# Kernel tuning notes

Measured on AMD Instinct MI355X. Metric: run time of the kernel, lower is better.

The kernel has to match this reference:

```python
import jax, jax.numpy as jnp
import numpy as np

N = 100000
E = 1600000
C_IN = 32
C_OUT = 64
DIM = 3
K = 2 ** DIM  # kernel_size=2 per pseudo-dim, degree=1 => 8 kernel slots
EPS = 1e-5

_BITS = jnp.asarray(np.array([[(c >> d) & 1 for d in range(DIM)] for c in range(K)], dtype=np.float32))  # [K,DIM]


def spline_basis(edge_attr):
    # edge_attr: [E,DIM] pseudo coords in [0,1]. kernel_size=2, degree=1 =>
    # per-dim linear basis (1-u, u); product over dims gives [E,K].
    u = edge_attr[:, None, :]            # [E,1,DIM]
    b = _BITS[None, :, :]                # [1,K,DIM]
    return jnp.prod(b * u + (1.0 - b) * (1.0 - u), axis=-1)  # [E,K]


def spline_conv(x, edge_index, edge_attr, W, W_root):
    # SplineConv with aggr='mean', root_weight=True, bias=False.
    src, dst = edge_index[0], edge_index[1]
    basis = spline_basis(edge_attr)                      # [E,K]
    x_j = x[src]                                         # [E,C_in] gather
    msg = jnp.einsum('ek,ei,kio->eo', basis, x_j, W)     # [E,C_out]
    agg = jax.ops.segment_sum(msg, dst, num_segments=N)  # [N,C_out] scatter-add
    cnt = jax.ops.segment_sum(jnp.ones((msg.shape[0],), msg.dtype), dst, num_segments=N)
    agg = agg / jnp.maximum(cnt, 1.0)[:, None]           # mean aggregation
    return agg + x @ W_root


def batch_norm(x, gamma, beta):
    mu = jnp.mean(x, axis=0)
    var = jnp.var(x, axis=0)
    return (x - mu) * jax.lax.rsqrt(var + EPS) * gamma + beta


def setup_inputs() -> dict:
    key = jax.random.key(0)
    ks = jax.random.split(key, 12)
    x = jax.random.normal(ks[0], (N, C_IN), jnp.float32)
    edge_index = jax.random.randint(ks[1], (2, E), 0, N, jnp.int32)
    edge_attr = jax.random.uniform(ks[2], (E, DIM), jnp.float32)
    s1 = 1.0 / np.sqrt(C_IN)
    s2 = 1.0 / np.sqrt(C_OUT)
    return {
        'x': x,
        'edge_index': edge_index,
        'edge_attr': edge_attr,
        'W1': jax.random.normal(ks[3], (K, C_IN, C_OUT), jnp.float32) * s1,
        'root1': jax.random.normal(ks[4], (C_IN, C_OUT), jnp.float32) * s1,
        'g1': jnp.ones((C_OUT,), jnp.float32),
        'b1': jnp.zeros((C_OUT,), jnp.float32),
        'W2': jax.random.normal(ks[5], (K, C_OUT, C_OUT), jnp.float32) * s2,
        'root2': jax.random.normal(ks[6], (C_OUT, C_OUT), jnp.float32) * s2,
        'g2': jnp.ones((C_OUT,), jnp.float32),
        'b2': jnp.zeros((C_OUT,), jnp.float32),
        'W_skip': jax.random.normal(ks[7], (C_IN, C_OUT), jnp.float32) * s1,
        'g_skip': jnp.ones((C_OUT,), jnp.float32),
        'b_skip': jnp.zeros((C_OUT,), jnp.float32),
    }


def reference(x, edge_index, edge_attr, W1, root1, g1, b1, W2, root2, g2, b2, W_skip, g_skip, b_skip):
    # ConvBlock: SplineConv -> BN -> elu
    h = spline_conv(x, edge_index, edge_attr, W1, root1)
    h = jax.nn.elu(batch_norm(h, g1, b1))
    # ConvBlockWithSkip: SplineConv -> BN; Linear skip -> BN; elu(sum)
    skip = batch_norm(x @ W_skip, g_skip, b_skip)
    h2 = batch_norm(spline_conv(h, edge_index, edge_attr, W2, root2), g2, b2)
    return jax.nn.elu(h2 + skip)
```

## Files before the change

### kernel.cpp

```cpp
#include <hip/hip_runtime.h>
#include <cstdint>

#define BN_EPS 1e-5f

typedef __attribute__((ext_vector_type(8))) short bf16x8;
typedef __attribute__((ext_vector_type(4))) float f32x4;
typedef __attribute__((ext_vector_type(2))) float f32x2;
typedef __attribute__((ext_vector_type(4))) unsigned int u32x4;
typedef unsigned int uint32;
typedef unsigned short u16;

__device__ inline u16 f2bf(float f) {
  unsigned int b = __float_as_uint(f);
  b += 0x7FFFu + ((b >> 16) & 1u);
  return (u16)(b >> 16);
}
__device__ inline float bf2f(u16 u) { return __uint_as_float((unsigned int)u << 16); }

__global__ __launch_bounds__(256) void prep(const float* __restrict__ W1,
                                            const float* __restrict__ root1,
                                            const float* __restrict__ Wskip,
                                            const float* __restrict__ W2,
                                            const float* __restrict__ root2,
                                            u16* __restrict__ B1t, u16* __restrict__ B2t,
                                            const float* __restrict__ x,
                                            u16* __restrict__ xbf, uint32* __restrict__ x8,
                                            int total8) {
  int idx = blockIdx.x * 256 + threadIdx.x;
  if (idx < 128 * 288) {
    int n = idx / 288, a = idx % 288;
    float v;
    if (a < 256) {
      int i = a >> 3, k = a & 7;
      v = (n < 64) ? W1[k * 2048 + i * 64 + n] : 0.f;
    } else {
      int i = a - 256;
      v = (n < 64) ? root1[i * 64 + n] : Wskip[i * 64 + (n - 64)];
    }
    B1t[idx] = f2bf(v);
  } else if (idx < 128 * 288 + 64 * 576) {
    int j = idx - 128 * 288;
    int n = j / 576, a = j % 576;
    float v;
    if (a < 512) {
      int i = a >> 3, k = a & 7;
      v = W2[k * 4096 + i * 64 + n];
    } else {
      v = root2[(a - 512) * 64 + n];
    }
    B2t[j] = f2bf(v);
  }
  if (idx < total8) {
    const float4* xp = (const float4*)x;
    float4 a = xp[2 * idx], b = xp[2 * idx + 1];
    union { u16 s[8]; uint4 u; } p;
    p.s[0] = f2bf(a.x); p.s[1] = f2bf(a.y); p.s[2] = f2bf(a.z); p.s[3] = f2bf(a.w);
    p.s[4] = f2bf(b.x); p.s[5] = f2bf(b.y); p.s[6] = f2bf(b.z); p.s[7] = f2bf(b.w);
    ((uint4*)xbf)[idx] = p.u;
    uint32 w0 = (uint32)__builtin_amdgcn_cvt_pk_fp8_f32(a.x, a.y, 0, false);
    w0 = (uint32)__builtin_amdgcn_cvt_pk_fp8_f32(a.z, a.w, (int)w0, true);
    uint32 w1 = (uint32)__builtin_amdgcn_cvt_pk_fp8_f32(b.x, b.y, 0, false);
    w1 = (uint32)__builtin_amdgcn_cvt_pk_fp8_f32(b.z, b.w, (int)w1, true);
    x8[2 * idx + 0] = w0;
    x8[2 * idx + 1] = w1;
  }
}

__global__ void hist_dst(const int* __restrict__ ei, int E, int* __restrict__ indeg,
                         int* __restrict__ rank) {
  int e = blockIdx.x * 256 + threadIdx.x;
  if (e >= E) return;
  rank[e] = atomicAdd(&indeg[ei[E + e]], 1);
}

__global__ __launch_bounds__(1024) void scan_block(const int* __restrict__ in,
                                                   int* __restrict__ part,
                                                   int* __restrict__ bsum, int N) {
  __shared__ int tmp[1024];
  int i = blockIdx.x * 1024 + threadIdx.x;
  int v = (i < N) ? in[i] : 0;
  tmp[threadIdx.x] = v;
  __syncthreads();
  for (int ofs = 1; ofs < 1024; ofs <<= 1) {
    int t = (threadIdx.x >= (unsigned)ofs) ? tmp[threadIdx.x - ofs] : 0;
    __syncthreads();
    tmp[threadIdx.x] += t;
    __syncthreads();
  }
  if (i < N) part[i] = tmp[threadIdx.x] - v;
  if (threadIdx.x == 1023) bsum[blockIdx.x] = tmp[1023];
}

__global__ __launch_bounds__(1024) void scan_top(int* __restrict__ bsum, int nb) {
  __shared__ int tmp[1024];
  int v = (threadIdx.x < (unsigned)nb) ? bsum[threadIdx.x] : 0;
  tmp[threadIdx.x] = v;
  __syncthreads();
  for (int ofs = 1; ofs < 1024; ofs <<= 1) {
    int t = (threadIdx.x >= (unsigned)ofs) ? tmp[threadIdx.x - ofs] : 0;
    __syncthreads();
    tmp[threadIdx.x] += t;
    __syncthreads();
  }
  if (threadIdx.x < (unsigned)nb) bsum[threadIdx.x] = tmp[threadIdx.x] - v;
}

__global__ void scan_add(const int* __restrict__ part, const int* __restrict__ bsum,
                         int* __restrict__ rowptr, int N, int E) {
  int i = blockIdx.x * 256 + threadIdx.x;
  if (i < N) rowptr[i] = part[i] + bsum[i >> 10];
  if (i == 0) rowptr[N] = E;
}

__global__ __launch_bounds__(256) void edge_scatter(const int* __restrict__ ei,
                                                    const float* __restrict__ attr,
                                                    const int* __restrict__ rowptr,
                                                    const int* __restrict__ rank, int E,
                                                    uint4* __restrict__ emeta) {
  int e = blockIdx.x * 256 + threadIdx.x;
  if (e >= E) return;
  int src = ei[e], dst = ei[E + e];
  union { _Float16 h[2]; uint32 u; } y, z;
  y.h[0] = (_Float16)attr[3 * e + 0];
  y.h[1] = (_Float16)attr[3 * e + 1];
  z.h[0] = (_Float16)attr[3 * e + 2];
  z.h[1] = (_Float16)0.f;
  int pos = rowptr[dst] + rank[e];
  emeta[pos] = make_uint4((uint32)src, y.u, z.u, 0u);
}

template <int PC, bool F8>
__device__ inline void sc_gather(const void* __restrict__ tab, int src, int p,
                                 f32x2* __restrict__ xf) {
  if (F8 && PC == 4) {
    uint32 u = *(const uint32*)((const char*)tab + (size_t)src * 64 + 4 * p);
    xf[0] = __builtin_amdgcn_cvt_pk_f32_fp8((int)u, false);
    xf[1] = __builtin_amdgcn_cvt_pk_f32_fp8((int)u, true);
  } else if (F8 && PC == 2) {
    u16 us = *(const u16*)((const char*)tab + (size_t)src * 32 + 2 * p);
    xf[0] = __builtin_amdgcn_cvt_pk_f32_fp8((int)us, false);
  } else {
    uint32 u = *(const uint32*)((const u16*)tab + (size_t)src * 32 + 2 * p);
    xf[0] = f32x2{__uint_as_float(u << 16), __uint_as_float(u & 0xFFFF0000u)};
  }
}

template <int PC>
__device__ inline void sc_fma(f32x2* __restrict__ acc2, u32x4 m,
                              const f32x2* __restrict__ xf) {
  union { uint32 u; _Float16 h[2]; } cy, cz;
  cy.u = m.y;
  cz.u = m.z;
  float u0 = (float)cy.h[0], u1 = (float)cy.h[1], u2 = (float)cz.h[0];
  float p0 = 1.f - u0, p1 = 1.f - u1, p2 = 1.f - u2;
  float w00 = p1 * p2, w10 = u1 * p2, w01 = p1 * u2, w11 = u1 * u2;
  float w[8] = {p0 * w00, u0 * w00, p0 * w10, u0 * w10,
                p0 * w01, u0 * w01, p0 * w11, u0 * w11};
#pragma unroll
  for (int k = 0; k < 8; k++) {
#pragma unroll
    for (int h = 0; h < PC / 2; h++) acc2[k * (PC / 2) + h] += xf[h] * w[k];
  }
}

template <int PC, bool F8>
__global__ __launch_bounds__(256) void msg_accum(const void* __restrict__ tab,
                                                 const int* __restrict__ rowptr,
                                                 const u32x4* __restrict__ emeta,
                                                 int n0, int n1, u16* __restrict__ T) {
  const int tid = threadIdx.x;
  const int lane = tid & 63;
  const int wv = tid >> 6;
  const int nwaves = gridDim.x * 4;
  const int p = lane & 15;
  const int eh = lane >> 4;
  const int PCH = PC / 2;

  for (int n = n0 + blockIdx.x * 4 + wv; n < n1; n += nwaves) {
    const int e0 = __builtin_amdgcn_readfirstlane(rowptr[n]);
    const int e1 = __builtin_amdgcn_readfirstlane(rowptr[n + 1]);
    f32x2 acc2[4 * PC];
#pragma unroll
    for (int j = 0; j < 4 * PC; j++) acc2[j] = f32x2{0.f, 0.f};

    int e = e0;
    for (; e + 8 <= e1; e += 8) {
      u32x4 a = __builtin_nontemporal_load(&emeta[e + eh]);
      u32x4 b = __builtin_nontemporal_load(&emeta[e + 4 + eh]);
      f32x2 xa[PC / 2], xb[PC / 2];
      sc_gather<PC, F8>(tab, (int)a.x, p, xa);
      sc_gather<PC, F8>(tab, (int)b.x, p, xb);
      sc_fma<PC>(acc2, a, xa);
      sc_fma<PC>(acc2, b, xb);
    }
    for (; e < e1; e += 4) {
      int ee = e + eh;
      bool act = ee < e1;
      if (!act) ee = e;
      u32x4 m = __builtin_nontemporal_load(&emeta[ee]);
      f32x2 xv[PC / 2];
      sc_gather<PC, F8>(tab, (int)m.x, p, xv);
      if (!act) {
#pragma unroll
        for (int h = 0; h < PC / 2; h++) xv[h] = f32x2{0.f, 0.f};
      }
      sc_fma<PC>(acc2, m, xv);
    }

#pragma unroll
    for (int j = 0; j < 4 * PC; j++) {
      f32x2 v = acc2[j];
      v.x += __shfl_xor(v.x, 16);
      v.x += __shfl_xor(v.x, 32);
      v.y += __shfl_xor(v.y, 16);
      v.y += __shfl_xor(v.y, 32);
      acc2[j] = v;
    }

    float inv = 1.f / fmaxf((float)(e1 - e0), 1.f);
    if (eh == 0) {
      u16* rowp = T + (size_t)(n - n0) * (128 * PC);
#pragma unroll
      for (int c = 0; c < PC; c++) {
        union { u16 s[8]; uint4 u; } pk;
#pragma unroll
        for (int k = 0; k < 8; k++) {
          f32x2 v = acc2[k * PCH + (c >> 1)];
          pk.s[k] = f2bf(((c & 1) ? v.y : v.x) * inv);
        }
        *(uint4*)(rowp + ((size_t)(PC * p + c)) * 8) = pk.u;
      }
    }
  }
}

template <int KT, int KX, int NC>
__global__ __launch_bounds__(256, 3) void gemm_agg(const u16* __restrict__ T,
                                                   const u16* __restrict__ X,
                                                   const u16* __restrict__ Bt,
                                                   u16* __restrict__ O1, u16* __restrict__ O2,
                                                   int rowOff, int rows,
                                                   double* __restrict__ sums) {
  const int K = KT + KX;
  const int KP = K + 8;
  const int NCH = NC / 2;
  const int tid = threadIdx.x;
  const int lane = tid & 63;
  const int wv = tid >> 6;
  const int rowbase = blockIdx.x * 64 + wv * 16;
  const int m = lane & 15;
  const int quad = lane >> 4;
  const int k0 = quad * 8;

  __shared__ u16 bs[NCH * (KT + KX + 8)];
  __shared__ float slds[4][NC][2];

  int ar = rowbase + m;
  if (ar > rows - 1) ar = rows - 1;

  bf16x8 afrag[K / 32];
#pragma unroll
  for (int f = 0; f < K / 32; f++) {
    if (f * 32 < KT)
      afrag[f] = *(const bf16x8*)(T + (size_t)ar * KT + f * 32 + k0);
    else
      afrag[f] = *(const bf16x8*)(X + (size_t)(rowOff + ar) * KX + (f * 32 - KT) + k0);
  }

  for (int halfc = 0; halfc < 2; halfc++) {
    __syncthreads();
    for (int i = tid; i < NCH * (K / 8); i += 256) {
      int col = i / (K / 8);
      int kk = (i % (K / 8)) * 8;
      *(uint4*)(bs + col * KP + kk) =
          *(const uint4*)(Bt + (size_t)(halfc * NCH + col) * K + kk);
    }
    __syncthreads();

    for (int col0 = 0; col0 < NCH; col0 += 32) {
      f32x4 acc0 = {0.f, 0.f, 0.f, 0.f};
      f32x4 acc1 = {0.f, 0.f, 0.f, 0.f};
#pragma unroll
      for (int f = 0; f < K / 32; f++) {
        bf16x8 b0 = *(const bf16x8*)(bs + (col0 + m) * KP + f * 32 + k0);
        bf16x8 b1 = *(const bf16x8*)(bs + (col0 + 16 + m) * KP + f * 32 + k0);
        acc0 = __builtin_amdgcn_mfma_f32_16x16x32_bf16(afrag[f], b0, acc0, 0, 0, 0);
        acc1 = __builtin_amdgcn_mfma_f32_16x16x32_bf16(afrag[f], b1, acc1, 0, 0, 0);
      }
#pragma unroll
      for (int half = 0; half < 2; half++) {
        const f32x4& acc = half ? acc1 : acc0;
        const int col = halfc * NCH + col0 + half * 16 + m;
        float s1 = 0.f, s2 = 0.f;
#pragma unroll
        for (int r = 0; r < 4; r++) {
          int gr = rowbase + quad * 4 + r;
          if (gr < rows) {
            size_t g = (size_t)(rowOff + gr);
            u16 vq = f2bf(acc[r]);
            float v = bf2f(vq);
            s1 += v;
            s2 += v * v;
            if (NC == 64 || col < 64) O1[g * 64 + col] = vq;
            else O2[g * 64 + (col - 64)] = vq;
          }
        }
        s1 += __shfl_xor(s1, 16); s1 += __shfl_xor(s1, 32);
        s2 += __shfl_xor(s2, 16); s2 += __shfl_xor(s2, 32);
        if (lane < 16) { slds[wv][col][0] = s1; slds[wv][col][1] = s2; }
      }
    }
  }
  __syncthreads();
  if (tid < NC * 2) {
    int col = tid >> 1, which = tid & 1;
    float v = slds[0][col][which] + slds[1][col][which] + slds[2][col][which] +
              slds[3][col][which];
    int slot = ((NC > 64 && col >= 64) ? 128 : 0) + which * 64 + (col & 63);
    atomicAdd(&sums[slot], (double)v);
  }
}

__global__ void bn_finalize2(const double* __restrict__ sums, const float* __restrict__ gA,
                             const float* __restrict__ bA, const float* __restrict__ gB,
                             const float* __restrict__ bB, float* __restrict__ scales, int N) {
  int t = threadIdx.x;
  int set = t >> 6, ch = t & 63;
  if (set == 1 && gB == nullptr) return;
  const float* g = set ? gB : gA;
  const float* b = set ? bB : bA;
  double mean = sums[set * 128 + ch] / (double)N;
  double var = sums[set * 128 + 64 + ch] / (double)N - mean * mean;
  double inv = 1.0 / sqrt(var + (double)BN_EPS);
  float sc = (float)((double)g[ch] * inv);
  scales[set * 128 + ch] = sc;
  scales[set * 128 + 64 + ch] = b[ch] - (float)mean * sc;
}

__global__ __launch_bounds__(256) void bn_elu_inplace(u16* __restrict__ h,
                                                      u16* __restrict__ h8,
                                                      const float* __restrict__ sc,
                                                      int total2) {
  int idx = blockIdx.x * 256 + threadIdx.x;
  if (idx >= total2) return;
  int ch = (idx * 2) & 63;
  uint32 u = ((const uint32*)h)[idx];
  float v0 = __uint_as_float(u << 16);
  float v1 = __uint_as_float(u & 0xFFFF0000u);
  v0 = v0 * sc[ch] + sc[64 + ch];
  v1 = v1 * sc[ch + 1] + sc[64 + ch + 1];
  v0 = v0 > 0.f ? v0 : expm1f(v0);
  v1 = v1 > 0.f ? v1 : expm1f(v1);
  ((uint32*)h)[idx] = ((uint32)f2bf(v1) << 16) | (uint32)f2bf(v0);
  int p8 = __builtin_amdgcn_cvt_pk_fp8_f32(v0, v1, 0, false);
  h8[idx] = (u16)(p8 & 0xFFFF);
}

__global__ __launch_bounds__(256) void final_k(const u16* __restrict__ h2pre,
                                               const u16* __restrict__ skip,
                                               const float* __restrict__ sc2,
                                               const float* __restrict__ scS,
                                               float* __restrict__ out, int total) {
  int idx = blockIdx.x * 256 + threadIdx.x;
  if (idx >= total) return;
  int ch = idx & 63;
  float h2 = bf2f(h2pre[idx]) * sc2[ch] + sc2[64 + ch];
  float s = bf2f(skip[idx]) * scS[ch] + scS[64 + ch];
  float v = h2 + s;
  out[idx] = v > 0.f ? v : expm1f(v);
}

extern "C" void kernel_launch(void* const* d_in, const int* in_sizes, int n_in,
                              void* d_out, int out_size, void* d_ws, size_t ws_size,
                              hipStream_t stream) {
  const float* x     = (const float*)d_in[0];
  const int*   ei    = (const int*)d_in[1];
  const float* attr  = (const float*)d_in[2];
  const float* W1    = (const float*)d_in[3];
  const float* root1 = (const float*)d_in[4];
  const float* g1    = (const float*)d_in[5];
  const float* b1    = (const float*)d_in[6];
  const float* W2    = (const float*)d_in[7];
  const float* root2 = (const float*)d_in[8];
  const float* g2    = (const float*)d_in[9];
  const float* b2    = (const float*)d_in[10];
  const float* Wskip = (const float*)d_in[11];
  const float* gS    = (const float*)d_in[12];
  const float* bS    = (const float*)d_in[13];
  const int N = in_sizes[0] / 32;
  const int E = in_sizes[1] / 2;
  const int Nh = (N + 1) / 2;
  float* out = (float*)d_out;

  char* ws = (char*)d_ws;
  size_t off = 0;
  auto alloc = [&](size_t bytes) {
    void* p = ws + off;
    off = (off + bytes + 255) & ~(size_t)255;
    return p;
  };
  u16* B1t = (u16*)alloc(128 * 288 * 2);
  u16* B2t = (u16*)alloc(64 * 576 * 2);
  double* sums = (double*)alloc(6 * 64 * 8);
  float* scales = (float*)alloc(6 * 64 * 4);
  int* indeg = (int*)alloc((size_t)N * 4);
  int* rowptr = (int*)alloc(((size_t)N + 1) * 4);
  int* part = (int*)alloc((size_t)N * 4);
  int* bsum = (int*)alloc(1024 * 4);
  int* rank = (int*)alloc((size_t)E * 4);
  uint4* emeta = (uint4*)alloc((size_t)E * 16);
  u16* xbf = (u16*)alloc((size_t)N * 32 * 2);
  uint32* x8 = (uint32*)alloc((size_t)N * 32);
  u16* h8 = (u16*)alloc((size_t)N * 64);
  u16* T = (u16*)alloc((size_t)(N + 2) * 256 * 2);
  u16* h1 = (u16*)alloc((size_t)N * 64 * 2);
  u16* skip = (u16*)alloc((size_t)N * 64 * 2);
  u16* h2 = (u16*)alloc((size_t)N * 64 * 2);
  if (off > ws_size) return;

  hipMemsetAsync(indeg, 0, (size_t)N * 4, stream);
  hipMemsetAsync(sums, 0, 6 * 64 * 8, stream);

  const int eblocks = (E + 255) / 256;
  const int nb = (N + 1023) / 1024;
  prep<<<(N * 4 + 255) / 256, 256, 0, stream>>>(W1, root1, Wskip, W2, root2, B1t, B2t,
                                                x, xbf, x8, N * 4);
  hist_dst<<<eblocks, 256, 0, stream>>>(ei, E, indeg, rank);
  scan_block<<<nb, 1024, 0, stream>>>(indeg, part, bsum, N);
  scan_top<<<1, 1024, 0, stream>>>(bsum, nb);
  scan_add<<<(N + 255) / 256, 256, 0, stream>>>(part, bsum, rowptr, N, E);
  edge_scatter<<<eblocks, 256, 0, stream>>>(ei, attr, rowptr, rank, E, emeta);

  msg_accum<2, true><<<2048, 256, 0, stream>>>(x8, rowptr, (const u32x4*)emeta, 0, N, T);
  gemm_agg<256, 32, 128><<<(N + 63) / 64, 256, 0, stream>>>(T, xbf, B1t, h1, skip, 0, N,
                                                            sums);
  bn_finalize2<<<1, 128, 0, stream>>>(sums, g1, b1, gS, bS, scales, N);
  bn_elu_inplace<<<(N * 32 + 255) / 256, 256, 0, stream>>>(h1, h8, scales, N * 32);

  for (int cph = 0; cph < 2; cph++) {
    int r0 = cph ? Nh : 0;
    int r1 = cph ? N : Nh;
    msg_accum<4, true><<<2048, 256, 0, stream>>>(h8, rowptr, (const u32x4*)emeta, r0, r1, T);
    gemm_agg<512, 64, 64><<<(r1 - r0 + 63) / 64, 256, 0, stream>>>(T, h1, B2t, h2, nullptr,
                                                                   r0, r1 - r0,
                                                                   sums + 4 * 64);
  }
  bn_finalize2<<<1, 64, 0, stream>>>(sums + 4 * 64, g2, b2, nullptr, nullptr,
                                     scales + 4 * 64, N);

  final_k<<<(N * 64 + 255) / 256, 256, 0, stream>>>(h2, skip, scales + 4 * 64,
                                                    scales + 2 * 64, out, N * 64);
}
```

Baseline: 568.2 us.

## Vectorize final kernel, drop nontemporal edge loads, raise layer-1 GEMM occupancy

The final BN+ELU kernel now processes two channels per thread, using 32-bit packed bf16 loads and float2 stores to halve the thread count and widen memory accesses. The edge metadata loads in msg_accum switch from nontemporal to regular loads so they may be cached. The layer-1 gemm_agg launch bound is raised to 4 waves per SIMD via a new template parameter, which may pressure registers.

```diff
diff --git a/kernel.cpp b/kernel.cpp
--- a/kernel.cpp
+++ b/kernel.cpp
@@ -185,8 +185,8 @@
 
     int e = e0;
     for (; e + 8 <= e1; e += 8) {
-      u32x4 a = __builtin_nontemporal_load(&emeta[e + eh]);
-      u32x4 b = __builtin_nontemporal_load(&emeta[e + 4 + eh]);
+      u32x4 a = emeta[e + eh];
+      u32x4 b = emeta[e + 4 + eh];
       f32x2 xa[PC / 2], xb[PC / 2];
       sc_gather<PC, F8>(tab, (int)a.x, p, xa);
       sc_gather<PC, F8>(tab, (int)b.x, p, xb);
@@ -197,7 +197,7 @@
       int ee = e + eh;
       bool act = ee < e1;
       if (!act) ee = e;
-      u32x4 m = __builtin_nontemporal_load(&emeta[ee]);
+      u32x4 m = emeta[ee];
       f32x2 xv[PC / 2];
       sc_gather<PC, F8>(tab, (int)m.x, p, xv);
       if (!act) {
@@ -234,13 +234,13 @@
   }
 }
 
-template <int KT, int KX, int NC>
-__global__ __launch_bounds__(256, 3) void gemm_agg(const u16* __restrict__ T,
-                                                   const u16* __restrict__ X,
-                                                   const u16* __restrict__ Bt,
-                                                   u16* __restrict__ O1, u16* __restrict__ O2,
-                                                   int rowOff, int rows,
-                                                   double* __restrict__ sums) {
+template <int KT, int KX, int NC, int MW>
+__global__ __launch_bounds__(256, MW) void gemm_agg(const u16* __restrict__ T,
+                                                    const u16* __restrict__ X,
+                                                    const u16* __restrict__ Bt,
+                                                    u16* __restrict__ O1, u16* __restrict__ O2,
+                                                    int rowOff, int rows,
+                                                    double* __restrict__ sums) {
   const int K = KT + KX;
   const int KP = K + 8;
   const int NCH = NC / 2;
@@ -360,14 +360,20 @@
                                                const u16* __restrict__ skip,
                                                const float* __restrict__ sc2,
                                                const float* __restrict__ scS,
-                                               float* __restrict__ out, int total) {
+                                               float* __restrict__ out, int total2) {
   int idx = blockIdx.x * 256 + threadIdx.x;
-  if (idx >= total) return;
-  int ch = idx & 63;
-  float h2 = bf2f(h2pre[idx]) * sc2[ch] + sc2[64 + ch];
-  float s = bf2f(skip[idx]) * scS[ch] + scS[64 + ch];
-  float v = h2 + s;
-  out[idx] = v > 0.f ? v : expm1f(v);
+  if (idx >= total2) return;
+  int ch = (idx * 2) & 63;
+  uint32 uh = ((const uint32*)h2pre)[idx];
+  uint32 us = ((const uint32*)skip)[idx];
+  float h20 = __uint_as_float(uh << 16) * sc2[ch] + sc2[64 + ch];
+  float h21 = __uint_as_float(uh & 0xFFFF0000u) * sc2[ch + 1] + sc2[64 + ch + 1];
+  float s0 = __uint_as_float(us << 16) * scS[ch] + scS[64 + ch];
+  float s1 = __uint_as_float(us & 0xFFFF0000u) * scS[ch + 1] + scS[64 + ch + 1];
+  float v0 = h20 + s0, v1 = h21 + s1;
+  v0 = v0 > 0.f ? v0 : expm1f(v0);
+  v1 = v1 > 0.f ? v1 : expm1f(v1);
+  ((float2*)out)[idx] = make_float2(v0, v1);
 }
 
 extern "C" void kernel_launch(void* const* d_in, const int* in_sizes, int n_in,
@@ -432,8 +438,8 @@
   edge_scatter<<<eblocks, 256, 0, stream>>>(ei, attr, rowptr, rank, E, emeta);
 
   msg_accum<2, true><<<2048, 256, 0, stream>>>(x8, rowptr, (const u32x4*)emeta, 0, N, T);
-  gemm_agg<256, 32, 128><<<(N + 63) / 64, 256, 0, stream>>>(T, xbf, B1t, h1, skip, 0, N,
-                                                            sums);
+  gemm_agg<256, 32, 128, 4><<<(N + 63) / 64, 256, 0, stream>>>(T, xbf, B1t, h1, skip, 0, N,
+                                                               sums);
   bn_finalize2<<<1, 128, 0, stream>>>(sums, g1, b1, gS, bS, scales, N);
   bn_elu_inplace<<<(N * 32 + 255) / 256, 256, 0, stream>>>(h1, h8, scales, N * 32);
 
@@ -441,13 +447,13 @@
     int r0 = cph ? Nh : 0;
     int r1 = cph ? N : Nh;
     msg_accum<4, true><<<2048, 256, 0, stream>>>(h8, rowptr, (const u32x4*)emeta, r0, r1, T);
-    gemm_agg<512, 64, 64><<<(r1 - r0 + 63) / 64, 256, 0, stream>>>(T, h1, B2t, h2, nullptr,
-                                                                   r0, r1 - r0,
-                                                                   sums + 4 * 64);
+    gemm_agg<512, 64, 64, 3><<<(r1 - r0 + 63) / 64, 256, 0, stream>>>(T, h1, B2t, h2,
+                                                                      nullptr, r0, r1 - r0,
+                                                                      sums + 4 * 64);
   }
   bn_finalize2<<<1, 64, 0, stream>>>(sums + 4 * 64, g2, b2, nullptr, nullptr,
                                      scales + 4 * 64, N);
 
-  final_k<<<(N * 64 + 255) / 256, 256, 0, stream>>>(h2, skip, scales + 4 * 64,
-                                                    scales + 2 * 64, out, N * 64);
-}
+  final_k<<<(N * 32 + 255) / 256, 256, 0, stream>>>(h2, skip, scales + 4 * 64,
+                                                    scales + 2 * 64, out, N * 32);
+}
```

Result: faster. 547.9 us (-3.6%).
